# Kernel optimization log

Hardware: AMD Instinct MI355X
Metric: run time of the kernel (lower is better)

The kernel has to match this reference:

```python
import math
import jax, jax.numpy as jnp
import numpy as np

N, M, DK, DV = 4096, 4096, 512, 512

def setup_inputs() -> dict:
    key = jax.random.key(0)
    k1, k2, k3, k4, k5 = jax.random.split(key, 5)
    return {
        "query": jax.random.normal(k1, (1, N, DK), dtype=jnp.float32),
        "q_k":   jax.random.normal(k2, (1, N, DK), dtype=jnp.float32),
        "q_v":   jax.random.normal(k3, (1, N, DV), dtype=jnp.float32),
        "key":   jax.random.normal(k4, (1, M, DK), dtype=jnp.float32),
        "value": jax.random.normal(k5, (1, M, DV), dtype=jnp.float32),
    }

def reference(query, q_k, q_v, key, value):
    dk = query.shape[-1]
    # diagonal of query[0] @ q_k[0].T without materializing the NxN product
    q_att = jnp.einsum('nd,nd->n', query[0], q_k[0])[:, None]      # [N, 1]
    scores = query[0] @ key[0].T                                    # [N, M]
    scores = jnp.concatenate([scores, q_att], axis=-1)[None]        # [1, N, M+1]
    scores = scores / math.sqrt(dk + 1)
    attention = jax.nn.softmax(scores, axis=-1)                     # [1, N, M+1]
    res = attention[:, :, :-1] @ value                              # [1, N, DV]
    return q_v * q_att + res
```

## Files before the change

kernel.cpp:

```cpp
#include <hip/hip_runtime.h>

#define NQ 4096
#define MK 4096
#define DKC 512
#define DVC 512
#define SCALE 0.044151079f

typedef __attribute__((ext_vector_type(8))) short short8;
typedef __attribute__((ext_vector_type(4))) float f32x4;

__device__ __forceinline__ unsigned short f2bf(float x) {
  unsigned u = __float_as_uint(x);
  u += 0x7fffu + ((u >> 16) & 1u);
  return (unsigned short)(u >> 16);
}
__device__ __forceinline__ float bf2f(unsigned short h) {
  return __uint_as_float((unsigned)h << 16);
}

#define GLL16(g, l)                                                        \
  __builtin_amdgcn_global_load_lds(                                        \
      (const __attribute__((address_space(1))) unsigned int*)(g),          \
      (__attribute__((address_space(3))) unsigned int*)(l), 16, 0, 0)

__global__ __launch_bounds__(256) void prep_all(const float* __restrict__ query,
                                                const float* __restrict__ q_k,
                                                const float* __restrict__ key,
                                                const float* __restrict__ value,
                                                unsigned short* __restrict__ Qb,
                                                unsigned short* __restrict__ Kb,
                                                unsigned short* __restrict__ Vt,
                                                float* __restrict__ qatt) {
  int b = blockIdx.x;
  if (b < 1024) {
    int n = b * 4 + (threadIdx.x >> 6);
    int lane = threadIdx.x & 63;
    const float4* qr = (const float4*)(query + (size_t)n * DKC + lane * 8);
    const float4* kr = (const float4*)(q_k + (size_t)n * DKC + lane * 8);
    float4 a0 = qr[0], a1 = qr[1];
    float4 b0 = kr[0], b1 = kr[1];
    float dot = a0.x * b0.x + a0.y * b0.y + a0.z * b0.z + a0.w * b0.w +
                a1.x * b1.x + a1.y * b1.y + a1.z * b1.z + a1.w * b1.w;
    unsigned short h[8] = {f2bf(a0.x * SCALE), f2bf(a0.y * SCALE), f2bf(a0.z * SCALE),
                           f2bf(a0.w * SCALE), f2bf(a1.x * SCALE), f2bf(a1.y * SCALE),
                           f2bf(a1.z * SCALE), f2bf(a1.w * SCALE)};
    *(short8*)(Qb + (size_t)n * DKC + lane * 8) = *(short8*)h;
#pragma unroll
    for (int off = 1; off < 64; off <<= 1) dot += __shfl_xor(dot, off, 64);
    if (lane == 0) qatt[n] = dot;
  } else if (b < 2048) {
    int i = (b - 1024) * 256 + threadIdx.x;
    const float4* src = (const float4*)key + (size_t)i * 2;
    float4 a0 = src[0], a1 = src[1];
    unsigned short h[8] = {f2bf(a0.x), f2bf(a0.y), f2bf(a0.z), f2bf(a0.w),
                           f2bf(a1.x), f2bf(a1.y), f2bf(a1.z), f2bf(a1.w)};
    *(short8*)(Kb + (size_t)i * 8) = *(short8*)h;
  } else {
    __shared__ float t[32][33];
    int bi = b - 2048;
    int tx = threadIdx.x & 31, ty = threadIdx.x >> 5;
    int m0 = (bi & 127) * 32;
    int d0 = (bi >> 7) * 32;
#pragma unroll
    for (int i = 0; i < 4; ++i)
      t[ty + i * 8][tx] = value[(size_t)(m0 + ty + i * 8) * DVC + d0 + tx];
    __syncthreads();
#pragma unroll
    for (int i = 0; i < 4; ++i)
      Vt[(size_t)(d0 + ty + i * 8) * MK + m0 + tx] = f2bf(t[tx][ty + i * 8]);
  }
}

__global__ __launch_bounds__(256, 3) void gemm_s(const unsigned short* __restrict__ Qb,
                                                 const unsigned short* __restrict__ Kb,
                                                 unsigned short* __restrict__ S) {
  __shared__ __align__(16) char lds[32768];
  const int tid = threadIdx.x;
  const int wid = tid >> 6, lane = tid & 63, lr = lane & 15, lh = lane >> 4;
  const int wm = wid >> 1, wn = wid & 1;

  int bid = blockIdx.x;
  int swz = (bid & 7) * 128 + (bid >> 3);
  const int tm = swz >> 5, tn = swz & 31;
  const size_t m0 = (size_t)tm * 128, n0 = (size_t)tn * 128;

  f32x4 acc[4][4];
#pragma unroll
  for (int i = 0; i < 4; ++i)
#pragma unroll
    for (int j = 0; j < 4; ++j) acc[i][j] = (f32x4){0.f, 0.f, 0.f, 0.f};

  const char* abase = (const char*)Qb + m0 * 1024;
  const char* bbase = (const char*)Kb + n0 * 1024;

  for (int ks = 0; ks < 8; ++ks) {
    const int kb = ks * 128;
    {
      char* al = lds;
      char* bl = lds + 16384;
#pragma unroll
      for (int s = 0; s < 4; ++s) {
        int obase = wid * 4096 + s * 1024;
        int o = obase + lane * 16;
        int row = o >> 7;
        int colg = ((o >> 4) & 7) ^ (row & 7);
        GLL16(abase + (size_t)row * 1024 + kb + colg * 16, al + obase);
        GLL16(bbase + (size_t)row * 1024 + kb + colg * 16, bl + obase);
      }
    }
    __syncthreads();
#pragma unroll
    for (int kk = 0; kk < 2; ++kk) {
      short8 af[4], bf[4];
#pragma unroll
      for (int i = 0; i < 4; ++i) {
        int ar = wm * 64 + i * 16 + lr;
        af[i] = *(const short8*)(lds + ar * 128 + ((((kk << 2) + lh) ^ (lr & 7)) << 4));
        int br = wn * 64 + i * 16 + lr;
        bf[i] = *(const short8*)(lds + 16384 + br * 128 + ((((kk << 2) + lh) ^ (lr & 7)) << 4));
      }
#pragma unroll
      for (int i = 0; i < 4; ++i)
#pragma unroll
        for (int j = 0; j < 4; ++j)
          acc[i][j] = __builtin_amdgcn_mfma_f32_16x16x32_bf16(af[i], bf[j], acc[i][j], 0, 0, 0);
    }
    __syncthreads();
  }

  unsigned short* sl = (unsigned short*)lds;
#pragma unroll
  for (int i = 0; i < 4; ++i)
#pragma unroll
    for (int j = 0; j < 4; ++j)
#pragma unroll
      for (int r = 0; r < 4; ++r) {
        int m = wm * 64 + i * 16 + lh * 4 + r;
        int n = wn * 64 + j * 16 + lr;
        sl[m * 128 + n] = f2bf(__expf(acc[i][j][r]));
      }
  __syncthreads();
#pragma unroll
  for (int i = 0; i < 8; ++i) {
    int o = i * 4096 + tid * 16;
    int row = o >> 8, colb = o & 255;
    *(uint4*)((char*)S + (m0 + row) * 8192 + n0 * 2 + colb) = *(const uint4*)((const char*)sl + o);
  }
}

__global__ __launch_bounds__(512, 1) void gemm_o_part(const unsigned short* __restrict__ P,
                                                      const unsigned short* __restrict__ Vt,
                                                      unsigned short* __restrict__ part) {
  __shared__ __align__(16) char lds[98304];
  const int tid = threadIdx.x;
  const int wid = tid >> 6, lane = tid & 63, lr = lane & 15, lh = lane >> 4;
  const int wm = wid >> 2, wn = wid & 3;

  int bid = blockIdx.x;
  int swz = (bid & 7) * 32 + (bid >> 3);
  const int ksl = swz & 3;
  const int nt = (swz >> 2) & 1;
  const int mt = swz >> 3;
  const size_t m0 = (size_t)mt * 128, n0 = (size_t)nt * 256;

  f32x4 acc[4][4];
#pragma unroll
  for (int i = 0; i < 4; ++i)
#pragma unroll
    for (int j = 0; j < 4; ++j) acc[i][j] = (f32x4){0.f, 0.f, 0.f, 0.f};

  const char* abase = (const char*)P + m0 * 8192 + (size_t)ksl * 2048;
  const char* bbase = (const char*)Vt + n0 * 8192 + (size_t)ksl * 2048;

  auto stage = [&](int ks, int b) {
    const int kb = ks * 128;
    char* al = lds + b * 49152;
    char* bl = al + 16384;
#pragma unroll
    for (int s = 0; s < 2; ++s) {
      int obase = wid * 2048 + s * 1024;
      int o = obase + lane * 16;
      int row = o >> 7;
      int colg = ((o >> 4) & 7) ^ (row & 7);
      GLL16(abase + (size_t)row * 8192 + kb + colg * 16, al + obase);
    }
#pragma unroll
    for (int s = 0; s < 4; ++s) {
      int obase = wid * 4096 + s * 1024;
      int o = obase + lane * 16;
      int row = o >> 7;
      int colg = ((o >> 4) & 7) ^ (row & 7);
      GLL16(bbase + (size_t)row * 8192 + kb + colg * 16, bl + obase);
    }
  };

  stage(0, 0);

  for (int ks = 0; ks < 16; ++ks) {
    const int cur = ks & 1;
    if (ks + 1 < 16) {
      stage(ks + 1, cur ^ 1);
      asm volatile("s_waitcnt vmcnt(6)" ::: "memory");
    } else {
      asm volatile("s_waitcnt vmcnt(0)" ::: "memory");
    }
    __builtin_amdgcn_s_barrier();
    asm volatile("" ::: "memory");

    const char* al = lds + cur * 49152;
    const char* bl = al + 16384;
#pragma unroll
    for (int kk = 0; kk < 2; ++kk) {
      short8 af[4], bf[4];
#pragma unroll
      for (int i = 0; i < 4; ++i) {
        int ar = wm * 64 + i * 16 + lr;
        af[i] = *(const short8*)(al + ar * 128 + ((((kk << 2) + lh) ^ (lr & 7)) << 4));
        int br = wn * 64 + i * 16 + lr;
        bf[i] = *(const short8*)(bl + br * 128 + ((((kk << 2) + lh) ^ (lr & 7)) << 4));
      }
#pragma unroll
      for (int i = 0; i < 4; ++i)
#pragma unroll
        for (int j = 0; j < 4; ++j)
          acc[i][j] = __builtin_amdgcn_mfma_f32_16x16x32_bf16(af[i], bf[j], acc[i][j], 0, 0, 0);
    }

    asm volatile("" ::: "memory");
    __builtin_amdgcn_s_barrier();
    asm volatile("" ::: "memory");
  }

  unsigned short* sl = (unsigned short*)lds;
#pragma unroll
  for (int i = 0; i < 4; ++i)
#pragma unroll
    for (int j = 0; j < 4; ++j)
#pragma unroll
      for (int r = 0; r < 4; ++r) {
        int m = wm * 64 + i * 16 + lh * 4 + r;
        int n = wn * 64 + j * 16 + lr;
        sl[m * 256 + n] = f2bf(acc[i][j][r]);
      }
  __builtin_amdgcn_s_barrier();
  asm volatile("" ::: "memory");
  char* pbase = (char*)part + (size_t)ksl * NQ * DVC * 2;
#pragma unroll
  for (int i = 0; i < 8; ++i) {
    int o = i * 8192 + tid * 16;
    int row = o >> 9, colb = o & 511;
    *(uint4*)(pbase + (m0 + row) * 1024 + n0 * 2 + colb) = *(const uint4*)((const char*)sl + o);
  }
}

__global__ __launch_bounds__(256) void combine_row(const unsigned short* __restrict__ Ppp,
                                                   const unsigned short* __restrict__ part,
                                                   const float* __restrict__ qatt,
                                                   const float* __restrict__ q_v,
                                                   float* __restrict__ out) {
  __shared__ float red[4];
  const int n = blockIdx.x;
  const int t = threadIdx.x;
  const int wv = t >> 6, lane = t & 63;
  const unsigned short* row = Ppp + (size_t)n * MK;
  short8 v0 = *(const short8*)(row + t * 16);
  short8 v1 = *(const short8*)(row + t * 16 + 8);
  float s = 0.f;
#pragma unroll
  for (int j = 0; j < 8; ++j) s += bf2f((unsigned short)v0[j]) + bf2f((unsigned short)v1[j]);
#pragma unroll
  for (int off = 1; off < 64; off <<= 1) s += __shfl_xor(s, off, 64);
  if (lane == 0) red[wv] = s;
  __syncthreads();
  float qa = qatt[n];
  float denom = red[0] + red[1] + red[2] + red[3] + __expf(qa * SCALE);
  float inv = 1.0f / denom;
  if (t < 64) {
    size_t off = (size_t)n * DVC + t * 8;
    float r[8] = {0.f, 0.f, 0.f, 0.f, 0.f, 0.f, 0.f, 0.f};
#pragma unroll
    for (int w = 0; w < 4; ++w) {
      short8 po = *(const short8*)(part + (size_t)w * NQ * DVC + off);
#pragma unroll
      for (int j = 0; j < 8; ++j) r[j] += bf2f((unsigned short)po[j]);
    }
    const float4* qv = (const float4*)(q_v + off);
    float4 qv0 = qv[0], qv1 = qv[1];
    float4 o0 = {qv0.x * qa + r[0] * inv, qv0.y * qa + r[1] * inv, qv0.z * qa + r[2] * inv,
                 qv0.w * qa + r[3] * inv};
    float4 o1 = {qv1.x * qa + r[4] * inv, qv1.y * qa + r[5] * inv, qv1.z * qa + r[6] * inv,
                 qv1.w * qa + r[7] * inv};
    float4* op = (float4*)(out + off);
    op[0] = o0;
    op[1] = o1;
  }
}

extern "C" void kernel_launch(void* const* d_in, const int* in_sizes, int n_in,
                              void* d_out, int out_size, void* d_ws, size_t ws_size,
                              hipStream_t stream) {
  const float* query = (const float*)d_in[0];
  const float* q_k = (const float*)d_in[1];
  const float* q_v = (const float*)d_in[2];
  const float* key = (const float*)d_in[3];
  const float* value = (const float*)d_in[4];
  float* out = (float*)d_out;

  char* ws = (char*)d_ws;
  unsigned short* Qb = (unsigned short*)(ws);
  unsigned short* Kb = (unsigned short*)(ws + (4u << 20));
  unsigned short* Vt = (unsigned short*)(ws + (8u << 20));
  unsigned short* S = (unsigned short*)(ws + (12u << 20));
  float* qatt = (float*)(ws + (44u << 20));
  unsigned short* part = (unsigned short*)(ws + (45u << 20));

  prep_all<<<dim3(4096), dim3(256), 0, stream>>>(query, q_k, key, value, Qb, Kb, Vt, qatt);
  gemm_s<<<dim3(1024), dim3(256), 0, stream>>>(Qb, Kb, S);
  gemm_o_part<<<dim3(256), dim3(512), 0, stream>>>(S, Vt, part);
  combine_row<<<dim3(4096), dim3(256), 0, stream>>>(S, part, qatt, q_v, out);
}
```

Baseline: 70.43 us.

## Fuse softmax row sums into score GEMM epilogue and split combine

The score GEMM epilogue now sums the fp32 exponentials of each row tile with warp shuffles and writes per-tile row partial sums. A small kernel reduces these into per-row inverse denominators. The combine kernel no longer re-reads the 32MB bf16 probability matrix and runs with all threads active. It adds one launch and a small LDS increase, raises the occupancy hint for gemm_s to 4, and now uses unrounded fp32 sums instead of sums of the bf16 values.

```diff
diff --git a/kernel.cpp b/kernel.cpp
--- a/kernel.cpp
+++ b/kernel.cpp
@@ -71,10 +71,11 @@
   }
 }
 
-__global__ __launch_bounds__(256, 3) void gemm_s(const unsigned short* __restrict__ Qb,
+__global__ __launch_bounds__(256, 4) void gemm_s(const unsigned short* __restrict__ Qb,
                                                  const unsigned short* __restrict__ Kb,
-                                                 unsigned short* __restrict__ S) {
-  __shared__ __align__(16) char lds[32768];
+                                                 unsigned short* __restrict__ S,
+                                                 float* __restrict__ rowsum_part) {
+  __shared__ __align__(16) char lds[33792];
   const int tid = threadIdx.x;
   const int wid = tid >> 6, lane = tid & 63, lr = lane & 15, lh = lane >> 4;
   const int wm = wid >> 1, wn = wid & 1;
@@ -129,6 +130,12 @@
   }
 
   unsigned short* sl = (unsigned short*)lds;
+  float* rs = (float*)(lds + 32768);
+  float rsum[4][4];
+#pragma unroll
+  for (int i = 0; i < 4; ++i)
+#pragma unroll
+    for (int r = 0; r < 4; ++r) rsum[i][r] = 0.f;
 #pragma unroll
   for (int i = 0; i < 4; ++i)
 #pragma unroll
@@ -137,9 +144,23 @@
       for (int r = 0; r < 4; ++r) {
         int m = wm * 64 + i * 16 + lh * 4 + r;
         int n = wn * 64 + j * 16 + lr;
-        sl[m * 128 + n] = f2bf(__expf(acc[i][j][r]));
-      }
+        float e = __expf(acc[i][j][r]);
+        sl[m * 128 + n] = f2bf(e);
+        rsum[i][r] += e;
+      }
+#pragma unroll
+  for (int i = 0; i < 4; ++i)
+#pragma unroll
+    for (int r = 0; r < 4; ++r) {
+      float v = rsum[i][r];
+      v += __shfl_xor(v, 1, 64);
+      v += __shfl_xor(v, 2, 64);
+      v += __shfl_xor(v, 4, 64);
+      v += __shfl_xor(v, 8, 64);
+      if (lr == 0) rs[wn * 128 + wm * 64 + i * 16 + lh * 4 + r] = v;
+    }
   __syncthreads();
+  if (tid < 128) rowsum_part[(size_t)tn * NQ + m0 + tid] = rs[tid] + rs[128 + tid];
 #pragma unroll
   for (int i = 0; i < 8; ++i) {
     int o = i * 4096 + tid * 16;
@@ -253,47 +274,43 @@
   }
 }
 
-__global__ __launch_bounds__(256) void combine_row(const unsigned short* __restrict__ Ppp,
-                                                   const unsigned short* __restrict__ part,
-                                                   const float* __restrict__ qatt,
-                                                   const float* __restrict__ q_v,
-                                                   float* __restrict__ out) {
-  __shared__ float red[4];
-  const int n = blockIdx.x;
-  const int t = threadIdx.x;
-  const int wv = t >> 6, lane = t & 63;
-  const unsigned short* row = Ppp + (size_t)n * MK;
-  short8 v0 = *(const short8*)(row + t * 16);
-  short8 v1 = *(const short8*)(row + t * 16 + 8);
+__global__ __launch_bounds__(256) void row_inv(const float* __restrict__ rowsum_part,
+                                               const float* __restrict__ qatt,
+                                               float* __restrict__ inv) {
+  int n = blockIdx.x * 256 + threadIdx.x;
   float s = 0.f;
 #pragma unroll
-  for (int j = 0; j < 8; ++j) s += bf2f((unsigned short)v0[j]) + bf2f((unsigned short)v1[j]);
-#pragma unroll
-  for (int off = 1; off < 64; off <<= 1) s += __shfl_xor(s, off, 64);
-  if (lane == 0) red[wv] = s;
-  __syncthreads();
+  for (int tn = 0; tn < 32; ++tn) s += rowsum_part[(size_t)tn * NQ + n];
+  inv[n] = 1.0f / (s + __expf(qatt[n] * SCALE));
+}
+
+__global__ __launch_bounds__(256) void combine2(const unsigned short* __restrict__ part,
+                                                const float* __restrict__ qatt,
+                                                const float* __restrict__ inv,
+                                                const float* __restrict__ q_v,
+                                                float* __restrict__ out) {
+  int idx = blockIdx.x * blockDim.x + threadIdx.x;
+  int n = idx >> 6;
+  int d8 = (idx & 63) * 8;
   float qa = qatt[n];
-  float denom = red[0] + red[1] + red[2] + red[3] + __expf(qa * SCALE);
-  float inv = 1.0f / denom;
-  if (t < 64) {
-    size_t off = (size_t)n * DVC + t * 8;
-    float r[8] = {0.f, 0.f, 0.f, 0.f, 0.f, 0.f, 0.f, 0.f};
-#pragma unroll
-    for (int w = 0; w < 4; ++w) {
-      short8 po = *(const short8*)(part + (size_t)w * NQ * DVC + off);
-#pragma unroll
-      for (int j = 0; j < 8; ++j) r[j] += bf2f((unsigned short)po[j]);
-    }
-    const float4* qv = (const float4*)(q_v + off);
-    float4 qv0 = qv[0], qv1 = qv[1];
-    float4 o0 = {qv0.x * qa + r[0] * inv, qv0.y * qa + r[1] * inv, qv0.z * qa + r[2] * inv,
-                 qv0.w * qa + r[3] * inv};
-    float4 o1 = {qv1.x * qa + r[4] * inv, qv1.y * qa + r[5] * inv, qv1.z * qa + r[6] * inv,
-                 qv1.w * qa + r[7] * inv};
-    float4* op = (float4*)(out + off);
-    op[0] = o0;
-    op[1] = o1;
-  }
+  float iv = inv[n];
+  size_t off = (size_t)n * DVC + d8;
+  float r[8] = {0.f, 0.f, 0.f, 0.f, 0.f, 0.f, 0.f, 0.f};
+#pragma unroll
+  for (int w = 0; w < 4; ++w) {
+    short8 po = *(const short8*)(part + (size_t)w * NQ * DVC + off);
+#pragma unroll
+    for (int j = 0; j < 8; ++j) r[j] += bf2f((unsigned short)po[j]);
+  }
+  const float4* qv = (const float4*)(q_v + off);
+  float4 qv0 = qv[0], qv1 = qv[1];
+  float4 o0 = {qv0.x * qa + r[0] * iv, qv0.y * qa + r[1] * iv, qv0.z * qa + r[2] * iv,
+               qv0.w * qa + r[3] * iv};
+  float4 o1 = {qv1.x * qa + r[4] * iv, qv1.y * qa + r[5] * iv, qv1.z * qa + r[6] * iv,
+               qv1.w * qa + r[7] * iv};
+  float4* op = (float4*)(out + off);
+  op[0] = o0;
+  op[1] = o1;
 }
 
 extern "C" void kernel_launch(void* const* d_in, const int* in_sizes, int n_in,
@@ -313,9 +330,12 @@
   unsigned short* S = (unsigned short*)(ws + (12u << 20));
   float* qatt = (float*)(ws + (44u << 20));
   unsigned short* part = (unsigned short*)(ws + (45u << 20));
+  float* rowsum_part = (float*)(ws + (61u << 20));
+  float* inv = (float*)(ws + (62u << 20));
 
   prep_all<<<dim3(4096), dim3(256), 0, stream>>>(query, q_k, key, value, Qb, Kb, Vt, qatt);
-  gemm_s<<<dim3(1024), dim3(256), 0, stream>>>(Qb, Kb, S);
+  gemm_s<<<dim3(1024), dim3(256), 0, stream>>>(Qb, Kb, S, rowsum_part);
   gemm_o_part<<<dim3(256), dim3(512), 0, stream>>>(S, Vt, part);
-  combine_row<<<dim3(4096), dim3(256), 0, stream>>>(S, part, qatt, q_v, out);
-}
+  row_inv<<<dim3(16), dim3(256), 0, stream>>>(rowsum_part, qatt, inv);
+  combine2<<<dim3(1024), dim3(256), 0, stream>>>(part, qatt, inv, q_v, out);
+}
```

New measurement: 68.16 us. 1.03x faster.
